# Optimization experiments

Measured on AMD Instinct MI355X. Metric: run time of the kernel, lower is better.

Reference implementation:

```python
import jax, jax.numpy as jnp
from jax import lax
import numpy as np

CLASS_NUMBER = 19
REGION_RADIUS = 1
KERNEL = 2 * REGION_RADIUS + 1  # 3
IMAGE_TOPK = 256
EPS = 1e-6


def setup_inputs() -> dict:
    key = jax.random.key(0)
    # softmax-like probabilities over classes
    raw = jax.random.uniform(key, (4, CLASS_NUMBER, 512, 1024), dtype=jnp.float32)
    logit = raw / jnp.sum(raw, axis=1, keepdims=True)
    return {"logit": logit}


def _box_sum(x):
    # kxk box sum with zero padding (SAME for odd kernel == pad=radius)
    return lax.reduce_window(x, jnp.float32(0), lax.add,
                             (1, 1, KERNEL, KERNEL), (1, 1, 1, 1), 'SAME')


def reference(logit):
    B, C, H, W = logit.shape
    logC = jnp.log(jnp.float32(C))

    # region uncertainty: normalized entropy, then avg-pool (count_include_pad)
    entropy = jnp.sum(-logit * jnp.log(logit + EPS), axis=1, keepdims=True) / logC
    region_uncertainty = _box_sum(entropy) / (KERNEL * KERNEL)  # [B,1,H,W]

    # region impurity: argmax -> one-hot -> depthwise box-sum (ones kernel)
    predict = jnp.argmax(logit, axis=1)                       # [B,H,W]
    one_hot = jax.nn.one_hot(predict, C, axis=1, dtype=logit.dtype)  # [B,C,H,W]
    summary = _box_sum(one_hot)                               # [B,C,H,W]
    count = jnp.sum(summary, axis=1, keepdims=True)           # [B,1,H,W]
    dist = summary / count
    region_impurity = jnp.sum(-dist * jnp.log(dist + EPS), axis=1, keepdims=True) / logC

    score = region_uncertainty * region_impurity              # [B,1,H,W]

    # per-image score: sum of top-k region scores
    flat = score.reshape(B, H * W)
    topk_vals, _ = lax.top_k(flat, IMAGE_TOPK)
    image_score = jnp.sum(topk_vals, axis=1)                  # [B]
    return image_score
```

## Files before the change

### kernel.cpp

```cpp
#include <hip/hip_runtime.h>
#include <cstdint>
#include <cstddef>

#define BB 4
#define CC 19
#define HH 512
#define WW 1024
#define HW (HH*WW)
#define HW4 (HW/4)
#define BHW (BB*HW)
#define KTOP 256
#define EPSF 1e-6f
#define NB1 8192
#define SEG 128
#define LOGC 2.9444389791664403f

__device__ __forceinline__ unsigned int sortable(float x) {
    unsigned int u = __float_as_uint(x);
    return (u & 0x80000000u) ? ~u : (u | 0x80000000u);
}
__device__ __forceinline__ float unsortable(unsigned int K) {
    unsigned int u = (K & 0x80000000u) ? (K & 0x7FFFFFFFu) : ~K;
    return __uint_as_float(u);
}

__global__ __launch_bounds__(256) void k_ent(const float4* __restrict__ logit,
                                             float4* __restrict__ ent,
                                             uchar4* __restrict__ pred,
                                             unsigned int* __restrict__ histz,
                                             float* __restrict__ outz) {
    int idx = blockIdx.x * 256 + threadIdx.x;
    if (idx < 98312) histz[idx] = 0;
    if (idx < BB) outz[idx] = 0.f;
    int b = idx >> 17;
    int q = idx & (HW4 - 1);
    const float4* base = logit + (size_t)b * CC * HW4 + q;
    float e0 = 0.f, e1 = 0.f, e2 = 0.f, e3 = 0.f;
    float m0 = -1.f, m1 = -1.f, m2 = -1.f, m3 = -1.f;
    int a0 = 0, a1 = 0, a2 = 0, a3 = 0;
#pragma unroll
    for (int c = 0; c < CC; ++c) {
        float4 p = base[(size_t)c * HW4];
        e0 -= p.x * __logf(p.x + EPSF); if (p.x > m0) { m0 = p.x; a0 = c; }
        e1 -= p.y * __logf(p.y + EPSF); if (p.y > m1) { m1 = p.y; a1 = c; }
        e2 -= p.z * __logf(p.z + EPSF); if (p.z > m2) { m2 = p.z; a2 = c; }
        e3 -= p.w * __logf(p.w + EPSF); if (p.w > m3) { m3 = p.w; a3 = c; }
    }
    ent[idx] = make_float4(e0, e1, e2, e3);
    pred[idx] = make_uchar4((unsigned char)a0, (unsigned char)a1,
                            (unsigned char)a2, (unsigned char)a3);
}

__global__ __launch_bounds__(256) void k_score_hist(const float* __restrict__ ent,
                                                    const unsigned char* __restrict__ pred,
                                                    float* __restrict__ score,
                                                    unsigned int* __restrict__ hist1) {
    __shared__ unsigned int lh[NB1];
    __shared__ float lgt[48];
    int b = blockIdx.x >> 7;
    int seg = blockIdx.x & (SEG - 1);
    for (int i = threadIdx.x; i < NB1; i += 256) lh[i] = 0;
    if (threadIdx.x < 48) {
        int nvi = threadIdx.x >> 4;
        int cnt = threadIdx.x & 15;
        float nv = (nvi == 0) ? 4.f : (nvi == 1) ? 6.f : 9.f;
        lgt[threadIdx.x] = __logf((float)cnt / nv + EPSF);
    }
    __syncthreads();
    const float* eb = ent + (size_t)b * HW;
    const unsigned char* pb = pred + (size_t)b * HW;
    int base = seg * (HW / SEG);

    for (int it = 0; it < 16; ++it) {
        int hw = base + it * 256 + threadIdx.x;
        int h = hw >> 10;
        int w = hw & (WW - 1);

        float es = 0.f;
        int cls[9];
        int nv = 0;
#pragma unroll
        for (int i = 0; i < 9; ++i) {
            int dh = i / 3 - 1, dw = i % 3 - 1;
            int hh = h + dh, ww = w + dw;
            bool ok = (hh >= 0) & (hh < HH) & (ww >= 0) & (ww < WW);
            int o = ok ? ((hh << 10) | ww) : 0;
            es += ok ? eb[o] : 0.f;
            cls[i] = ok ? (int)pb[o] : 255;
            nv += ok ? 1 : 0;
        }
        float inv = 1.f / (float)nv;
        int nvi = (nv == 9) ? 2 : ((nv == 6) ? 1 : 0);
        const float* lg = &lgt[nvi * 16];
        float lsum = 0.f;
#pragma unroll
        for (int i = 0; i < 9; ++i) {
            int cnt = 0;
#pragma unroll
            for (int j = 0; j < 9; ++j) cnt += (cls[j] == cls[i]) ? 1 : 0;
            float lv = lg[cnt];
            lsum += (cls[i] != 255) ? lv : 0.f;
        }
        float imp = -inv * lsum;
        float v = (es * (1.f / (9.f * LOGC))) * (imp * (1.f / LOGC));
        score[(size_t)b * HW + hw] = v;
        atomicAdd(&lh[sortable(v) >> 19], 1u);
    }
    __syncthreads();
    unsigned int* hb = hist1 + (size_t)b * NB1;
    for (int i = threadIdx.x; i < NB1; i += 256) {
        unsigned int c = lh[i];
        if (c) atomicAdd(&hb[i], c);
    }
}

__device__ __forceinline__ void select_bin(const unsigned int* __restrict__ hb,
                                           int rem, int* bin_out, int* rem_out) {
    __shared__ unsigned int cs[256];
    __shared__ unsigned int bs[32];
    __shared__ int s_chunk, s_bin, s_rem;
    int t = threadIdx.x;
    unsigned int s = 0;
#pragma unroll 8
    for (int i = 0; i < 32; ++i) s += hb[t * 32 + i];
    cs[t] = s;
    __syncthreads();
    for (int d = 1; d < 256; d <<= 1) {
        unsigned int v = (t + d < 256) ? cs[t + d] : 0;
        __syncthreads();
        cs[t] += v;
        __syncthreads();
    }
    unsigned int St = cs[t];
    unsigned int St1 = (t < 255) ? cs[t + 1] : 0;
    if ((int)St >= rem && (t == 255 || (int)St1 < rem)) {
        s_chunk = t;
        s_rem = rem - (int)St1;
    }
    __syncthreads();
    int chunk = s_chunk;
    int rem2 = s_rem;
    if (t < 32) bs[t] = hb[chunk * 32 + t];
    __syncthreads();
    for (int d = 1; d < 32; d <<= 1) {
        unsigned int v = (t < 32 && t + d < 32) ? bs[t + d] : 0;
        __syncthreads();
        if (t < 32) bs[t] += v;
        __syncthreads();
    }
    if (t < 32) {
        unsigned int Sb = bs[t];
        unsigned int Sb1 = (t < 31) ? bs[t + 1] : 0;
        if ((int)Sb >= rem2 && (t == 31 || (int)Sb1 < rem2)) {
            s_bin = chunk * 32 + t;
            s_rem = rem2 - (int)Sb1;
        }
    }
    __syncthreads();
    *bin_out = s_bin;
    *rem_out = s_rem;
}

__global__ __launch_bounds__(256) void k_scan1(const unsigned int* __restrict__ hist1,
                                               unsigned int* __restrict__ T1,
                                               int* __restrict__ r1) {
    int b = blockIdx.x;
    int bin, rem;
    select_bin(hist1 + (size_t)b * NB1, KTOP, &bin, &rem);
    if (threadIdx.x == 0) { T1[b] = (unsigned int)bin; r1[b] = rem; }
}

__global__ __launch_bounds__(256) void k_hist2(const float4* __restrict__ score,
                                               const unsigned int* __restrict__ T1,
                                               unsigned int* __restrict__ hist2,
                                               float* __restrict__ hsum,
                                               float* __restrict__ out) {
    __shared__ unsigned int lh[NB1];
    __shared__ float ls[NB1];
    __shared__ float red[4];
    int b = blockIdx.x >> 7;
    int seg = blockIdx.x & (SEG - 1);
    for (int i = threadIdx.x; i < NB1; i += 256) { lh[i] = 0; ls[i] = 0.f; }
    __syncthreads();
    unsigned int t1 = T1[b];
    const float4* p = score + ((size_t)b * HW + (size_t)seg * (HW / SEG)) / 4;
    float sa = 0.f;
    for (int i = threadIdx.x; i < (HW / SEG) / 4; i += 256) {
        float4 v = p[i];
        float vv[4] = {v.x, v.y, v.z, v.w};
#pragma unroll
        for (int q = 0; q < 4; ++q) {
            unsigned int k = sortable(vv[q]);
            unsigned int cb = k >> 19;
            if (cb > t1) sa += vv[q];
            else if (cb == t1) {
                int sub = (k >> 6) & 0x1FFF;
                atomicAdd(&lh[sub], 1u);
                atomicAdd(&ls[sub], vv[q]);
            }
        }
    }
    __syncthreads();
    unsigned int* hb = hist2 + (size_t)b * NB1;
    float* sb = hsum + (size_t)b * NB1;
    for (int i = threadIdx.x; i < NB1; i += 256) {
        unsigned int c = lh[i];
        if (c) { atomicAdd(&hb[i], c); atomicAdd(&sb[i], ls[i]); }
    }
#pragma unroll
    for (int d = 32; d; d >>= 1) sa += __shfl_down(sa, d);
    if ((threadIdx.x & 63) == 0) red[threadIdx.x >> 6] = sa;
    __syncthreads();
    if (threadIdx.x == 0) {
        float tt = red[0] + red[1] + red[2] + red[3];
        if (tt != 0.f) atomicAdd(&out[b], tt);
    }
}

__global__ __launch_bounds__(256) void k_scan2(const unsigned int* __restrict__ hist2,
                                               const float* __restrict__ hsum,
                                               const unsigned int* __restrict__ T1,
                                               const int* __restrict__ r1,
                                               float* __restrict__ out) {
    int b = blockIdx.x;
    int bin, rem;
    select_bin(hist2 + (size_t)b * NB1, r1[b], &bin, &rem);
    __shared__ float rs[256];
    int t = threadIdx.x;
    const float* sb = hsum + (size_t)b * NB1;
    float s = 0.f;
    for (int i = t; i < NB1; i += 256) if (i > bin) s += sb[i];
    rs[t] = s;
    __syncthreads();
    for (int d = 128; d; d >>= 1) {
        if (t < d) rs[t] += rs[t + d];
        __syncthreads();
    }
    if (t == 0) {
        unsigned int K = (T1[b] << 19) | ((unsigned int)bin << 6);
        out[b] += rs[0] + unsortable(K) * (float)rem;
    }
}

extern "C" void kernel_launch(void* const* d_in, const int* in_sizes, int n_in,
                              void* d_out, int out_size, void* d_ws, size_t ws_size,
                              hipStream_t stream) {
    const float* logit = (const float*)d_in[0];
    float* out = (float*)d_out;
    char* ws = (char*)d_ws;

    float*         ent   = (float*)(ws);
    unsigned char* pred  = (unsigned char*)(ws + 8388608);
    float*         score = (float*)(ws + 10485760);
    unsigned int*  histb = (unsigned int*)(ws + 18874368);
    unsigned int*  hist1 = histb;
    unsigned int*  hist2 = histb + 32768;
    float*         hsum  = (float*)(histb + 65536);
    unsigned int*  T1    = histb + 98304;
    int*           r1    = (int*)(histb + 98308);

    k_ent<<<BHW / 4 / 256, 256, 0, stream>>>((const float4*)logit, (float4*)ent,
                                             (uchar4*)pred, histb, out);
    k_score_hist<<<BB * SEG, 256, 0, stream>>>(ent, pred, score, hist1);
    k_scan1<<<BB, 256, 0, stream>>>(hist1, T1, r1);
    k_hist2<<<BB * SEG, 256, 0, stream>>>((const float4*)score, T1, hist2, hsum, out);
    k_scan2<<<BB, 256, 0, stream>>>(hist2, hsum, T1, r1, out);
}
```

Baseline: 292.9 us.

## Stage stencil rows in LDS and fold first scan into second histogram pass

The score kernel now loads a 6-row halo tile of entropy and prediction into shared memory with zero/255 padding, so the 3x3 neighbourhood reads come from LDS instead of repeated global loads with bounds checks. The first-level histogram shrinks to 4096 bins, and the separate scan1 launch is removed. Instead, every k_hist2 block redundantly computes the threshold bin from hist1. This saves one kernel launch and the LDS clear work, at the cost of more shared memory per block and redundant scan work in 512 blocks.

```diff
diff --git a/kernel.cpp b/kernel.cpp
--- a/kernel.cpp
+++ b/kernel.cpp
@@ -11,8 +11,10 @@
 #define BHW (BB*HW)
 #define KTOP 256
 #define EPSF 1e-6f
-#define NB1 8192
+#define NB1 4096
+#define NB2 8192
 #define SEG 128
+#define LSTRIDE 1032
 #define LOGC 2.9444389791664403f
 
 __device__ __forceinline__ unsigned int sortable(float x) {
@@ -30,7 +32,7 @@
                                              unsigned int* __restrict__ histz,
                                              float* __restrict__ outz) {
     int idx = blockIdx.x * 256 + threadIdx.x;
-    if (idx < 98312) histz[idx] = 0;
+    if (idx < 81928) histz[idx] = 0;
     if (idx < BB) outz[idx] = 0.f;
     int b = idx >> 17;
     int q = idx & (HW4 - 1);
@@ -55,40 +57,54 @@
                                                     const unsigned char* __restrict__ pred,
                                                     float* __restrict__ score,
                                                     unsigned int* __restrict__ hist1) {
+    __shared__ __align__(16) float ent_s[6 * LSTRIDE];
+    __shared__ __align__(16) unsigned char pred_s[6 * LSTRIDE];
     __shared__ unsigned int lh[NB1];
     __shared__ float lgt[48];
+    int tid = threadIdx.x;
     int b = blockIdx.x >> 7;
     int seg = blockIdx.x & (SEG - 1);
-    for (int i = threadIdx.x; i < NB1; i += 256) lh[i] = 0;
-    if (threadIdx.x < 48) {
-        int nvi = threadIdx.x >> 4;
-        int cnt = threadIdx.x & 15;
+    int r0 = seg * 4;
+
+    for (int i = tid; i < 6 * LSTRIDE; i += 256) { ent_s[i] = 0.f; pred_s[i] = 255; }
+    for (int i = tid; i < NB1; i += 256) lh[i] = 0;
+    if (tid < 48) {
+        int nvi = tid >> 4, cnt = tid & 15;
         float nv = (nvi == 0) ? 4.f : (nvi == 1) ? 6.f : 9.f;
-        lgt[threadIdx.x] = __logf((float)cnt / nv + EPSF);
-    }
-    __syncthreads();
+        lgt[tid] = __logf((float)cnt / nv + EPSF);
+    }
+    __syncthreads();
+
     const float* eb = ent + (size_t)b * HW;
     const unsigned char* pb = pred + (size_t)b * HW;
-    int base = seg * (HW / SEG);
-
+    for (int i = tid; i < 1536; i += 256) {
+        int rr = i >> 8, c4 = i & 255;
+        int g = r0 - 1 + rr;
+        if (g >= 0 && g < HH) {
+            float4 v = *(const float4*)(eb + g * WW + c4 * 4);
+            *(float4*)&ent_s[rr * LSTRIDE + 4 + c4 * 4] = v;
+            uchar4 pv = *(const uchar4*)(pb + g * WW + c4 * 4);
+            *(uchar4*)&pred_s[rr * LSTRIDE + 4 + c4 * 4] = pv;
+        }
+    }
+    __syncthreads();
+
+    float* sbuf = score + (size_t)b * HW;
+#pragma unroll
     for (int it = 0; it < 16; ++it) {
-        int hw = base + it * 256 + threadIdx.x;
-        int h = hw >> 10;
-        int w = hw & (WW - 1);
-
+        int p = it * 256 + tid;
+        int py = p >> 10, px = p & 1023;
+        int h = r0 + py, w = px;
+        int l0 = py * LSTRIDE + 3 + px;
         float es = 0.f;
         int cls[9];
-        int nv = 0;
 #pragma unroll
         for (int i = 0; i < 9; ++i) {
-            int dh = i / 3 - 1, dw = i % 3 - 1;
-            int hh = h + dh, ww = w + dw;
-            bool ok = (hh >= 0) & (hh < HH) & (ww >= 0) & (ww < WW);
-            int o = ok ? ((hh << 10) | ww) : 0;
-            es += ok ? eb[o] : 0.f;
-            cls[i] = ok ? (int)pb[o] : 255;
-            nv += ok ? 1 : 0;
-        }
+            int o = l0 + (i / 3) * LSTRIDE + (i % 3);
+            es += ent_s[o];
+            cls[i] = pred_s[o];
+        }
+        int nv = ((h > 0) + (h < HH - 1) + 1) * ((w > 0) + (w < WW - 1) + 1);
         float inv = 1.f / (float)nv;
         int nvi = (nv == 9) ? 2 : ((nv == 6) ? 1 : 0);
         const float* lg = &lgt[nvi * 16];
@@ -103,19 +119,63 @@
         }
         float imp = -inv * lsum;
         float v = (es * (1.f / (9.f * LOGC))) * (imp * (1.f / LOGC));
-        score[(size_t)b * HW + hw] = v;
-        atomicAdd(&lh[sortable(v) >> 19], 1u);
+        sbuf[h * WW + w] = v;
+        atomicAdd(&lh[sortable(v) >> 20], 1u);
     }
     __syncthreads();
     unsigned int* hb = hist1 + (size_t)b * NB1;
-    for (int i = threadIdx.x; i < NB1; i += 256) {
+    for (int i = tid; i < NB1; i += 256) {
         unsigned int c = lh[i];
         if (c) atomicAdd(&hb[i], c);
     }
 }
 
-__device__ __forceinline__ void select_bin(const unsigned int* __restrict__ hb,
-                                           int rem, int* bin_out, int* rem_out) {
+__device__ __forceinline__ void select4k(const unsigned int* __restrict__ hb,
+                                         int rem, int* bin_out, int* rem_out) {
+    __shared__ unsigned int cs[256];
+    __shared__ unsigned int bs[16];
+    __shared__ int s_chunk, s_bin, s_rem;
+    int t = threadIdx.x;
+    unsigned int s = 0;
+#pragma unroll
+    for (int i = 0; i < 16; ++i) s += hb[t * 16 + i];
+    cs[t] = s;
+    __syncthreads();
+    for (int d = 1; d < 256; d <<= 1) {
+        unsigned int v = (t + d < 256) ? cs[t + d] : 0;
+        __syncthreads();
+        cs[t] += v;
+        __syncthreads();
+    }
+    unsigned int St = cs[t];
+    unsigned int St1 = (t < 255) ? cs[t + 1] : 0;
+    if ((int)St >= rem && (t == 255 || (int)St1 < rem)) {
+        s_chunk = t; s_rem = rem - (int)St1;
+    }
+    __syncthreads();
+    int chunk = s_chunk, rem2 = s_rem;
+    if (t < 16) bs[t] = hb[chunk * 16 + t];
+    __syncthreads();
+    for (int d = 1; d < 16; d <<= 1) {
+        unsigned int v = (t < 16 && t + d < 16) ? bs[t + d] : 0;
+        __syncthreads();
+        if (t < 16) bs[t] += v;
+        __syncthreads();
+    }
+    if (t < 16) {
+        unsigned int Sb = bs[t];
+        unsigned int Sb1 = (t < 15) ? bs[t + 1] : 0;
+        if ((int)Sb >= rem2 && (t == 15 || (int)Sb1 < rem2)) {
+            s_bin = chunk * 16 + t; s_rem = rem2 - (int)Sb1;
+        }
+    }
+    __syncthreads();
+    *bin_out = s_bin;
+    *rem_out = s_rem;
+}
+
+__device__ __forceinline__ void select8k(const unsigned int* __restrict__ hb,
+                                         int rem, int* bin_out, int* rem_out) {
     __shared__ unsigned int cs[256];
     __shared__ unsigned int bs[32];
     __shared__ int s_chunk, s_bin, s_rem;
@@ -134,12 +194,10 @@
     unsigned int St = cs[t];
     unsigned int St1 = (t < 255) ? cs[t + 1] : 0;
     if ((int)St >= rem && (t == 255 || (int)St1 < rem)) {
-        s_chunk = t;
-        s_rem = rem - (int)St1;
-    }
-    __syncthreads();
-    int chunk = s_chunk;
-    int rem2 = s_rem;
+        s_chunk = t; s_rem = rem - (int)St1;
+    }
+    __syncthreads();
+    int chunk = s_chunk, rem2 = s_rem;
     if (t < 32) bs[t] = hb[chunk * 32 + t];
     __syncthreads();
     for (int d = 1; d < 32; d <<= 1) {
@@ -152,8 +210,7 @@
         unsigned int Sb = bs[t];
         unsigned int Sb1 = (t < 31) ? bs[t + 1] : 0;
         if ((int)Sb >= rem2 && (t == 31 || (int)Sb1 < rem2)) {
-            s_bin = chunk * 32 + t;
-            s_rem = rem2 - (int)Sb1;
+            s_bin = chunk * 32 + t; s_rem = rem2 - (int)Sb1;
         }
     }
     __syncthreads();
@@ -161,28 +218,24 @@
     *rem_out = s_rem;
 }
 
-__global__ __launch_bounds__(256) void k_scan1(const unsigned int* __restrict__ hist1,
-                                               unsigned int* __restrict__ T1,
-                                               int* __restrict__ r1) {
-    int b = blockIdx.x;
-    int bin, rem;
-    select_bin(hist1 + (size_t)b * NB1, KTOP, &bin, &rem);
-    if (threadIdx.x == 0) { T1[b] = (unsigned int)bin; r1[b] = rem; }
-}
-
 __global__ __launch_bounds__(256) void k_hist2(const float4* __restrict__ score,
-                                               const unsigned int* __restrict__ T1,
+                                               const unsigned int* __restrict__ hist1,
                                                unsigned int* __restrict__ hist2,
                                                float* __restrict__ hsum,
+                                               unsigned int* __restrict__ T1g,
+                                               int* __restrict__ r1g,
                                                float* __restrict__ out) {
-    __shared__ unsigned int lh[NB1];
-    __shared__ float ls[NB1];
+    __shared__ unsigned int lh[NB2];
+    __shared__ float ls[NB2];
     __shared__ float red[4];
     int b = blockIdx.x >> 7;
     int seg = blockIdx.x & (SEG - 1);
-    for (int i = threadIdx.x; i < NB1; i += 256) { lh[i] = 0; ls[i] = 0.f; }
-    __syncthreads();
-    unsigned int t1 = T1[b];
+    int bin1, rem1;
+    select4k(hist1 + (size_t)b * NB1, KTOP, &bin1, &rem1);
+    unsigned int t1 = (unsigned int)bin1;
+    if (seg == 0 && threadIdx.x == 0) { T1g[b] = t1; r1g[b] = rem1; }
+    for (int i = threadIdx.x; i < NB2; i += 256) { lh[i] = 0; ls[i] = 0.f; }
+    __syncthreads();
     const float4* p = score + ((size_t)b * HW + (size_t)seg * (HW / SEG)) / 4;
     float sa = 0.f;
     for (int i = threadIdx.x; i < (HW / SEG) / 4; i += 256) {
@@ -191,19 +244,19 @@
 #pragma unroll
         for (int q = 0; q < 4; ++q) {
             unsigned int k = sortable(vv[q]);
-            unsigned int cb = k >> 19;
+            unsigned int cb = k >> 20;
             if (cb > t1) sa += vv[q];
             else if (cb == t1) {
-                int sub = (k >> 6) & 0x1FFF;
+                int sub = (k >> 7) & 0x1FFF;
                 atomicAdd(&lh[sub], 1u);
                 atomicAdd(&ls[sub], vv[q]);
             }
         }
     }
     __syncthreads();
-    unsigned int* hb = hist2 + (size_t)b * NB1;
-    float* sb = hsum + (size_t)b * NB1;
-    for (int i = threadIdx.x; i < NB1; i += 256) {
+    unsigned int* hb = hist2 + (size_t)b * NB2;
+    float* sb = hsum + (size_t)b * NB2;
+    for (int i = threadIdx.x; i < NB2; i += 256) {
         unsigned int c = lh[i];
         if (c) { atomicAdd(&hb[i], c); atomicAdd(&sb[i], ls[i]); }
     }
@@ -219,17 +272,17 @@
 
 __global__ __launch_bounds__(256) void k_scan2(const unsigned int* __restrict__ hist2,
                                                const float* __restrict__ hsum,
-                                               const unsigned int* __restrict__ T1,
-                                               const int* __restrict__ r1,
+                                               const unsigned int* __restrict__ T1g,
+                                               const int* __restrict__ r1g,
                                                float* __restrict__ out) {
     int b = blockIdx.x;
     int bin, rem;
-    select_bin(hist2 + (size_t)b * NB1, r1[b], &bin, &rem);
+    select8k(hist2 + (size_t)b * NB2, r1g[b], &bin, &rem);
     __shared__ float rs[256];
     int t = threadIdx.x;
-    const float* sb = hsum + (size_t)b * NB1;
+    const float* sb = hsum + (size_t)b * NB2;
     float s = 0.f;
-    for (int i = t; i < NB1; i += 256) if (i > bin) s += sb[i];
+    for (int i = t; i < NB2; i += 256) if (i > bin) s += sb[i];
     rs[t] = s;
     __syncthreads();
     for (int d = 128; d; d >>= 1) {
@@ -237,7 +290,7 @@
         __syncthreads();
     }
     if (t == 0) {
-        unsigned int K = (T1[b] << 19) | ((unsigned int)bin << 6);
+        unsigned int K = (T1g[b] << 20) | ((unsigned int)bin << 7);
         out[b] += rs[0] + unsortable(K) * (float)rem;
     }
 }
@@ -254,15 +307,15 @@
     float*         score = (float*)(ws + 10485760);
     unsigned int*  histb = (unsigned int*)(ws + 18874368);
     unsigned int*  hist1 = histb;
-    unsigned int*  hist2 = histb + 32768;
-    float*         hsum  = (float*)(histb + 65536);
-    unsigned int*  T1    = histb + 98304;
-    int*           r1    = (int*)(histb + 98308);
+    unsigned int*  hist2 = histb + 16384;
+    float*         hsum  = (float*)(histb + 49152);
+    unsigned int*  T1g   = histb + 81920;
+    int*           r1g   = (int*)(histb + 81924);
 
     k_ent<<<BHW / 4 / 256, 256, 0, stream>>>((const float4*)logit, (float4*)ent,
                                              (uchar4*)pred, histb, out);
     k_score_hist<<<BB * SEG, 256, 0, stream>>>(ent, pred, score, hist1);
-    k_scan1<<<BB, 256, 0, stream>>>(hist1, T1, r1);
-    k_hist2<<<BB * SEG, 256, 0, stream>>>((const float4*)score, T1, hist2, hsum, out);
-    k_scan2<<<BB, 256, 0, stream>>>(hist2, hsum, T1, r1, out);
-}
+    k_hist2<<<BB * SEG, 256, 0, stream>>>((const float4*)score, hist1,
+                                          hist2, hsum, T1g, r1g, out);
+    k_scan2<<<BB, 256, 0, stream>>>(hist2, hsum, T1g, r1g, out);
+}
```

Result: no change. 288.2 us (-1.6%).
